# Kernel optimization log

Measured on AMD Instinct MI355X. Metric: run time of the kernel, lower is better.

## Reference

```python
import jax, jax.numpy as jnp
import numpy as np
import math

IN_FEATURES = 4096
OUT_FEATURES = 4096
TOKENS = 8192


def hydrate_weight(seed, out_features, in_features):
    """Deterministically synthesize the virtual weight matrix from the 64-bit seed.
    Mirrors nn.Linear's kaiming-uniform-style bound (1/sqrt(fan_in)) used by gmem_rs
    hydration; never stored as a parameter."""
    bound = 1.0 / math.sqrt(in_features)
    key = jax.random.key(seed)
    return jax.random.uniform(
        key, (out_features, in_features), dtype=jnp.float32,
        minval=-bound, maxval=bound)


def setup_inputs() -> dict:
    key = jax.random.key(0)
    kx, kb = jax.random.split(key)
    x = jax.random.normal(kx, (TOKENS, IN_FEATURES), dtype=jnp.float32)
    bound = 1.0 / math.sqrt(IN_FEATURES)
    bias = jax.random.uniform(kb, (OUT_FEATURES,), dtype=jnp.float32,
                              minval=-bound, maxval=bound)
    return {"x": x, "bias": bias, "seed": 1140071481}


def reference(x, bias, seed):
    # Hydrate weight on-the-fly from seed (zero-RAM virtual weight), then GEMM.
    W = hydrate_weight(seed, OUT_FEATURES, IN_FEATURES)  # [out, in]
    y = jnp.einsum('ti,oi->to', x, W)  # [tokens, out]
    return y + bias
```

## Files before the change

kernel.cpp:

```cpp
#include <hip/hip_runtime.h>
#include <hip/hip_bf16.h>
#include <stdint.h>

#define TOKENS 8192
#define NOUT   4096
#define KIN    4096

#define BM 256
#define BN 256
#define BK 64
#define NT (KIN / BK)

typedef __attribute__((ext_vector_type(8))) short bf16x8;
typedef __attribute__((ext_vector_type(4))) float f32x4;

__device__ __forceinline__ uint32_t rotl32(uint32_t x, int r) {
  return (x << r) | (x >> (32 - r));
}

__device__ __forceinline__ uint16_t f2bf_rne(float f) {
  uint32_t u = __float_as_uint(f);
  u += 0x7FFFu + ((u >> 16) & 1u);
  return (uint16_t)(u >> 16);
}

__device__ __forceinline__ void threefry2x32(uint32_t k0, uint32_t k1,
                                             uint32_t c0, uint32_t c1,
                                             uint32_t& o0, uint32_t& o1) {
  uint32_t ks2 = 0x1BD11BDAu ^ k0 ^ k1;
  uint32_t x0 = c0 + k0;
  uint32_t x1 = c1 + k1;
#define TFR(r) { x0 += x1; x1 = rotl32(x1, (r)); x1 ^= x0; }
  TFR(13) TFR(15) TFR(26) TFR(6)
  x0 += k1;  x1 += ks2 + 1u;
  TFR(17) TFR(29) TFR(16) TFR(24)
  x0 += ks2; x1 += k0 + 2u;
  TFR(13) TFR(15) TFR(26) TFR(6)
  x0 += k0;  x1 += k1 + 3u;
  TFR(17) TFR(29) TFR(16) TFR(24)
  x0 += k1;  x1 += ks2 + 4u;
  TFR(13) TFR(15) TFR(26) TFR(6)
  x0 += ks2; x1 += k0 + 5u;
#undef TFR
  o0 = x0; o1 = x1;
}

__global__ void prep_kernel(const float* __restrict__ x,
                            uint16_t* __restrict__ xb,
                            uint16_t* __restrict__ W,
                            const int* __restrict__ seed_ptr) {
  uint32_t b = blockIdx.x;
  if (b < 65536u) {
    uint32_t k1 = (uint32_t)(*seed_ptr);
    uint32_t j = b * 256u + threadIdx.x;
    uint32_t o0, o1;
    threefry2x32(0u, k1, 0u, j, o0, o1);
    uint32_t bits = o0 ^ o1;
    const float scale = 0.03125f;
    const float mn    = -0.015625f;
    float f = __uint_as_float((bits >> 9) | 0x3F800000u) - 1.0f;
    float v = fmaxf(mn, f * scale + mn);
    W[j] = f2bf_rne(v);
  } else {
    uint32_t base = ((b - 65536u) * 256u + threadIdx.x) * 8u;
    f32x4 a = *(const f32x4*)(x + base);
    f32x4 c = *(const f32x4*)(x + base + 4);
    union { uint16_t u[8]; bf16x8 v; } r;
    r.u[0] = f2bf_rne(a[0]); r.u[1] = f2bf_rne(a[1]);
    r.u[2] = f2bf_rne(a[2]); r.u[3] = f2bf_rne(a[3]);
    r.u[4] = f2bf_rne(c[0]); r.u[5] = f2bf_rne(c[1]);
    r.u[6] = f2bf_rne(c[2]); r.u[7] = f2bf_rne(c[3]);
    *(bf16x8*)(xb + base) = r.v;
  }
}

__global__ __launch_bounds__(512, 2)
void gemm_bias_kernel(const uint16_t* __restrict__ A,
                      const uint16_t* __restrict__ B,
                      const float* __restrict__ bias,
                      float* __restrict__ C) {
  __shared__ uint16_t smem[2][2][16384];

  const int nwgn = NOUT / BN;
  const int nwg  = (TOKENS / BM) * nwgn;
  int bid = blockIdx.x;
  int cpx = nwg >> 3;
  int swzb = (bid & 7) * cpx + (bid >> 3);
  int tm = (swzb / nwgn) * BM;
  int tn = (swzb % nwgn) * BN;

  const int t    = threadIdx.x;
  const int lane = t & 63;
  const int wid  = t >> 6;
  const int wm   = wid >> 2;
  const int wn   = wid & 3;
  const int fr   = lane & 15;
  const int fq   = lane >> 4;

  const int swzRd = (lane & 7) << 4;
  const int lsw   = ((lane & 7) ^ (lane >> 3)) << 4;

  f32x4 acc[8][4] = {};

  auto stageHalf = [&](int mat, int h, int kt, int buf) {
    const uint16_t* g = mat ? B : A;
    const int rb = (mat ? tn : tm) + h * 128 + wid * 16 + (lane >> 3);
    const char* src = (const char*)(g + (size_t)rb * KIN) + kt * 128 + lsw;
    char* dst = (char*)&smem[buf][mat][0] + h * 16384 + wid * 2048 + lane * 16;
#pragma unroll
    for (int q = 0; q < 2; ++q) {
      __builtin_amdgcn_global_load_lds(
          (const __attribute__((address_space(1))) void*)(src + (size_t)q * 8 * KIN * 2),
          (__attribute__((address_space(3))) void*)(dst + q * 1024),
          16, 0, 0);
    }
  };

#define VMW(N) asm volatile("s_waitcnt vmcnt(" #N ")" ::: "memory")
#define LKW(N) asm volatile("s_waitcnt lgkmcnt(" #N ")" ::: "memory")

#define RD_A(Ab, MH)                                                           \
    _Pragma("unroll")                                                          \
    for (int s = 0; s < 2; ++s) {                                              \
      const int kb = (s << 6) | (fq << 4);                                     \
      _Pragma("unroll")                                                        \
      for (int i = 0; i < 4; ++i)                                              \
        af[s][i] = *(const bf16x8*)((Ab) +                                     \
            (wm * 64 + (MH) * 128 + i * 16 + fr) * 128 + (kb ^ swzRd));        \
    }

#define RD_B(Bb, BV, NH)                                                       \
    _Pragma("unroll")                                                          \
    for (int s = 0; s < 2; ++s) {                                              \
      const int kb = (s << 6) | (fq << 4);                                     \
      _Pragma("unroll")                                                        \
      for (int j = 0; j < 2; ++j)                                              \
        BV[s][j] = *(const bf16x8*)((Bb) +                                     \
            (wn * 32 + (NH) * 128 + j * 16 + fr) * 128 + (kb ^ swzRd));        \
    }

#define MFCL(MH, NH, BV)                                                       \
    __builtin_amdgcn_s_barrier();                                              \
    asm volatile("s_waitcnt lgkmcnt(0)" ::: "memory");                         \
    __builtin_amdgcn_sched_barrier(0);                                         \
    __builtin_amdgcn_s_setprio(1);                                             \
    _Pragma("unroll")                                                          \
    for (int s = 0; s < 2; ++s)                                                \
      _Pragma("unroll")                                                        \
      for (int i = 0; i < 4; ++i)                                              \
        _Pragma("unroll")                                                      \
        for (int j = 0; j < 2; ++j)                                            \
          acc[(MH) * 4 + i][(NH) * 2 + j] =                                    \
              __builtin_amdgcn_mfma_f32_16x16x32_bf16(                         \
                  af[s][i], BV[s][j], acc[(MH) * 4 + i][(NH) * 2 + j], 0, 0, 0); \
    __builtin_amdgcn_s_setprio(0);                                             \
    __builtin_amdgcn_s_barrier();

#define KTILE(BUF, KT, MODE)                                                   \
  {                                                                            \
    bf16x8 af[2][4], bv0[2][2], bv1[2][2];                                     \
    const char* Ab = (const char*)&smem[BUF][0][0];                            \
    const char* Bb = (const char*)&smem[BUF][1][0];                            \
                              \
    RD_A(Ab, 0) RD_B(Bb, bv0, 0)                                               \
    if ((MODE) <= 1) stageHalf(0, 1, (KT) + 1, (BUF) ^ 1);                     \
    LKW(8);                                                                    \
    MFCL(0, 0, bv0)                                                            \
                                    \
    RD_B(Bb, bv1, 1)                                                           \
    if ((MODE) == 0) stageHalf(0, 0, (KT) + 2, (BUF));                         \
    MFCL(0, 1, bv1)                                                            \
                                    \
    RD_A(Ab, 1)                                                                \
    if ((MODE) == 0) stageHalf(1, 0, (KT) + 2, (BUF));                         \
    MFCL(1, 1, bv1)                                                            \
            \
    if ((MODE) == 0) stageHalf(1, 1, (KT) + 2, (BUF));                         \
    if ((MODE) == 0) { VMW(6); } else if ((MODE) == 1) { VMW(0); }             \
    MFCL(1, 0, bv0)                                                            \
  }

  stageHalf(0, 0, 0, 0); stageHalf(1, 0, 0, 0);
  stageHalf(0, 1, 0, 0); stageHalf(1, 1, 0, 0);
  VMW(4);
  stageHalf(0, 0, 1, 1); stageHalf(1, 0, 1, 1); stageHalf(1, 1, 1, 1);
  VMW(6);
  __builtin_amdgcn_s_barrier();

  for (int kt = 0; kt < NT - 2; kt += 2) {
    KTILE(0, kt, 0)
    KTILE(1, kt + 1, 0)
  }
  KTILE(0, 62, 1)
  KTILE(1, 63, 2)

#undef KTILE
#undef MFCL
#undef RD_B
#undef RD_A
#undef LKW
#undef VMW

#pragma unroll
  for (int nj = 0; nj < 4; ++nj) {
    const int nh = nj >> 1, j = nj & 1;
    const int col = tn + wn * 32 + nh * 128 + j * 16 + fr;
    const float bvs = bias[col];
#pragma unroll
    for (int mi = 0; mi < 8; ++mi) {
      const int mh = mi >> 2, i = mi & 3;
      const int row0 = tm + wm * 64 + mh * 128 + i * 16 + fq * 4;
#pragma unroll
      for (int rr = 0; rr < 4; ++rr)
        C[(size_t)(row0 + rr) * NOUT + col] = acc[mi][nj][rr] + bvs;
    }
  }
}

extern "C" void kernel_launch(void* const* d_in, const int* in_sizes, int n_in,
                              void* d_out, int out_size, void* d_ws, size_t ws_size,
                              hipStream_t stream) {
  const float* x    = (const float*)d_in[0];
  const float* bias = (const float*)d_in[1];
  const int*   seed = (const int*)d_in[2];
  float* y = (float*)d_out;

  uint16_t* Wb = (uint16_t*)d_ws;
  uint16_t* Xb = Wb + (size_t)NOUT * KIN;

  prep_kernel<<<65536 + 16384, 256, 0, stream>>>(x, Xb, Wb, seed);

  const int grid = (TOKENS / BM) * (NOUT / BN);
  gemm_bias_kernel<<<grid, 512, 0, stream>>>(Xb, Wb, bias, y);
}
```

Before: 284.1 us.

## Switch GEMM inner loop to 32x32x16 MFMA with split LDS reads

Replaces the 16x16x32 bf16 MFMA tiles with 32x32x16 MFMAs, so each wave issues fewer, larger matrix instructions and needs fewer LDS fragment reads per k-tile. LDS reads are split into two halves with partial lgkmcnt waits, so the first MFMA batch can start before all fragments arrive. The accumulator layout and epilogue indexing are remapped to the 32x32 output layout. The extra barriers and the changed register footprint could reduce overlap or occupancy.

```diff
diff --git a/kernel.cpp b/kernel.cpp
--- a/kernel.cpp
+++ b/kernel.cpp
@@ -11,8 +11,9 @@
 #define BK 64
 #define NT (KIN / BK)
 
-typedef __attribute__((ext_vector_type(8))) short bf16x8;
-typedef __attribute__((ext_vector_type(4))) float f32x4;
+typedef __attribute__((ext_vector_type(8)))  short bf16x8;
+typedef __attribute__((ext_vector_type(4)))  float f32x4;
+typedef __attribute__((ext_vector_type(16))) float f32x16;
 
 __device__ __forceinline__ uint32_t rotl32(uint32_t x, int r) {
   return (x << r) | (x >> (32 - r));
@@ -94,13 +95,13 @@
   const int wid  = t >> 6;
   const int wm   = wid >> 2;
   const int wn   = wid & 3;
-  const int fr   = lane & 15;
-  const int fq   = lane >> 4;
+  const int rrow = lane & 31;
+  const int khi  = (lane >> 5) << 4;
 
   const int swzRd = (lane & 7) << 4;
   const int lsw   = ((lane & 7) ^ (lane >> 3)) << 4;
 
-  f32x4 acc[8][4] = {};
+  f32x16 acc[4][2] = {};
 
   auto stageHalf = [&](int mat, int h, int kt, int buf) {
     const uint16_t* g = mat ? B : A;
@@ -118,66 +119,71 @@
 
 #define VMW(N) asm volatile("s_waitcnt vmcnt(" #N ")" ::: "memory")
 #define LKW(N) asm volatile("s_waitcnt lgkmcnt(" #N ")" ::: "memory")
-
-#define RD_A(Ab, MH)                                                           \
+#define SB0    __builtin_amdgcn_sched_barrier(0)
+#define PRI(p) __builtin_amdgcn_s_setprio(p)
+
+#define RD_A2(Ab, MH, S)                                                       \
     _Pragma("unroll")                                                          \
-    for (int s = 0; s < 2; ++s) {                                              \
-      const int kb = (s << 6) | (fq << 4);                                     \
+    for (int ss = 0; ss < 2; ++ss)                                             \
       _Pragma("unroll")                                                        \
-      for (int i = 0; i < 4; ++i)                                              \
-        af[s][i] = *(const bf16x8*)((Ab) +                                     \
-            (wm * 64 + (MH) * 128 + i * 16 + fr) * 128 + (kb ^ swzRd));        \
-    }
-
-#define RD_B(Bb, BV, NH)                                                       \
+      for (int i2 = 0; i2 < 2; ++i2)                                           \
+        af[(S) + ss][i2] = *(const bf16x8*)((Ab) +                             \
+            (wm * 64 + (MH) * 128 + i2 * 32 + rrow) * 128 +                    \
+            (((((S) + ss) << 5) + khi) ^ swzRd));
+
+#define RD_B2(Bb, BV, NH, S)                                                   \
     _Pragma("unroll")                                                          \
-    for (int s = 0; s < 2; ++s) {                                              \
-      const int kb = (s << 6) | (fq << 4);                                     \
+    for (int ss = 0; ss < 2; ++ss)                                             \
+      BV[(S) + ss] = *(const bf16x8*)((Bb) +                                   \
+          (wn * 32 + (NH) * 128 + rrow) * 128 +                                \
+          (((((S) + ss) << 5) + khi) ^ swzRd));
+
+#define MF4(MH, NH, BV, S)                                                     \
+    _Pragma("unroll")                                                          \
+    for (int ss = 0; ss < 2; ++ss)                                             \
       _Pragma("unroll")                                                        \
-      for (int j = 0; j < 2; ++j)                                              \
-        BV[s][j] = *(const bf16x8*)((Bb) +                                     \
-            (wn * 32 + (NH) * 128 + j * 16 + fr) * 128 + (kb ^ swzRd));        \
-    }
-
-#define MFCL(MH, NH, BV)                                                       \
-    __builtin_amdgcn_s_barrier();                                              \
-    asm volatile("s_waitcnt lgkmcnt(0)" ::: "memory");                         \
-    __builtin_amdgcn_sched_barrier(0);                                         \
-    __builtin_amdgcn_s_setprio(1);                                             \
-    _Pragma("unroll")                                                          \
-    for (int s = 0; s < 2; ++s)                                                \
-      _Pragma("unroll")                                                        \
-      for (int i = 0; i < 4; ++i)                                              \
-        _Pragma("unroll")                                                      \
-        for (int j = 0; j < 2; ++j)                                            \
-          acc[(MH) * 4 + i][(NH) * 2 + j] =                                    \
-              __builtin_amdgcn_mfma_f32_16x16x32_bf16(                         \
-                  af[s][i], BV[s][j], acc[(MH) * 4 + i][(NH) * 2 + j], 0, 0, 0); \
-    __builtin_amdgcn_s_setprio(0);                                             \
-    __builtin_amdgcn_s_barrier();
+      for (int i2 = 0; i2 < 2; ++i2)                                           \
+        acc[(MH) * 2 + i2][NH] = __builtin_amdgcn_mfma_f32_32x32x16_bf16(      \
+            af[(S) + ss][i2], BV[(S) + ss], acc[(MH) * 2 + i2][NH], 0, 0, 0);
 
 #define KTILE(BUF, KT, MODE)                                                   \
   {                                                                            \
-    bf16x8 af[2][4], bv0[2][2], bv1[2][2];                                     \
+    bf16x8 af[4][2], bv0[4], bv1[4];                                           \
     const char* Ab = (const char*)&smem[BUF][0][0];                            \
     const char* Bb = (const char*)&smem[BUF][1][0];                            \
-                              \
-    RD_A(Ab, 0) RD_B(Bb, bv0, 0)                                               \
+                  \
+    RD_A2(Ab, 0, 0) RD_B2(Bb, bv0, 0, 0)                                       \
+    SB0;                                                                       \
+    RD_A2(Ab, 0, 2) RD_B2(Bb, bv0, 0, 2)                                       \
     if ((MODE) <= 1) stageHalf(0, 1, (KT) + 1, (BUF) ^ 1);                     \
-    LKW(8);                                                                    \
-    MFCL(0, 0, bv0)                                                            \
-                                    \
-    RD_B(Bb, bv1, 1)                                                           \
+    __builtin_amdgcn_s_barrier();                                              \
+    LKW(6); SB0; PRI(1); MF4(0, 0, bv0, 0)                                     \
+    LKW(0); SB0; MF4(0, 0, bv0, 2) PRI(0);                                     \
+    __builtin_amdgcn_s_barrier();                                              \
+                       \
+    RD_B2(Bb, bv1, 1, 0)                                                       \
+    SB0;                                                                       \
+    RD_B2(Bb, bv1, 1, 2)                                                       \
     if ((MODE) == 0) stageHalf(0, 0, (KT) + 2, (BUF));                         \
-    MFCL(0, 1, bv1)                                                            \
-                                    \
-    RD_A(Ab, 1)                                                                \
+    __builtin_amdgcn_s_barrier();                                              \
+    LKW(2); SB0; PRI(1); MF4(0, 1, bv1, 0)                                     \
+    LKW(0); SB0; MF4(0, 1, bv1, 2) PRI(0);                                     \
+    __builtin_amdgcn_s_barrier();                                              \
+       \
+    RD_A2(Ab, 1, 0)                                                            \
+    SB0;                                                                       \
+    RD_A2(Ab, 1, 2)                                                            \
     if ((MODE) == 0) stageHalf(1, 0, (KT) + 2, (BUF));                         \
-    MFCL(1, 1, bv1)                                                            \
-            \
+    __builtin_amdgcn_s_barrier();                                              \
+    LKW(4); SB0; PRI(1); MF4(1, 1, bv1, 0)                                     \
+    LKW(0); SB0; MF4(1, 1, bv1, 2) PRI(0);                                     \
+    __builtin_amdgcn_s_barrier();                                              \
+       \
     if ((MODE) == 0) stageHalf(1, 1, (KT) + 2, (BUF));                         \
     if ((MODE) == 0) { VMW(6); } else if ((MODE) == 1) { VMW(0); }             \
-    MFCL(1, 0, bv0)                                                            \
+    __builtin_amdgcn_s_barrier();                                              \
+    PRI(1); MF4(1, 0, bv0, 0) MF4(1, 0, bv0, 2) PRI(0);                        \
+    __builtin_amdgcn_s_barrier();                                              \
   }
 
   stageHalf(0, 0, 0, 0); stageHalf(1, 0, 0, 0);
@@ -195,24 +201,27 @@
   KTILE(1, 63, 2)
 
 #undef KTILE
-#undef MFCL
-#undef RD_B
-#undef RD_A
+#undef MF4
+#undef RD_B2
+#undef RD_A2
+#undef PRI
+#undef SB0
 #undef LKW
 #undef VMW
 
 #pragma unroll
-  for (int nj = 0; nj < 4; ++nj) {
-    const int nh = nj >> 1, j = nj & 1;
-    const int col = tn + wn * 32 + nh * 128 + j * 16 + fr;
+  for (int nh = 0; nh < 2; ++nh) {
+    const int col = tn + wn * 32 + nh * 128 + rrow;
     const float bvs = bias[col];
 #pragma unroll
-    for (int mi = 0; mi < 8; ++mi) {
-      const int mh = mi >> 2, i = mi & 3;
-      const int row0 = tm + wm * 64 + mh * 128 + i * 16 + fq * 4;
-#pragma unroll
-      for (int rr = 0; rr < 4; ++rr)
-        C[(size_t)(row0 + rr) * NOUT + col] = acc[mi][nj][rr] + bvs;
+    for (int mi2 = 0; mi2 < 4; ++mi2) {
+      const int mh = mi2 >> 1, i2 = mi2 & 1;
+      const int row0 = tm + wm * 64 + mh * 128 + i2 * 32 + ((lane >> 5) << 2);
+#pragma unroll
+      for (int r = 0; r < 16; ++r) {
+        const int row = row0 + (r & 3) + 8 * (r >> 2);
+        C[(size_t)row * NOUT + col] = acc[mi2][nh][r] + bvs;
+      }
     }
   }
 }
```

After: 307.9 us. +8.4%, slower.

## Prefetch next k-tile's first LDS fragments during last MFMA cluster

Applied to the files above, without the earlier changes.

Restructures the per-k-tile schedule so the A/B fragments for the next tile's first MFMA cluster are read from LDS while the current tile's last cluster runs, with fragments held in persistent registers across tiles. It also reorders the MFMA quadrants and tunes lgkmcnt waits so LDS reads overlap the matrix-core work instead of stalling before each cluster. The cost is more live vector registers (two A and two B fragment sets), which may lower occupancy or cause spills, and the prologue now waits for all initial loads.

```diff
diff --git a/kernel.cpp b/kernel.cpp
--- a/kernel.cpp
+++ b/kernel.cpp
@@ -118,74 +118,79 @@
 
 #define VMW(N) asm volatile("s_waitcnt vmcnt(" #N ")" ::: "memory")
 #define LKW(N) asm volatile("s_waitcnt lgkmcnt(" #N ")" ::: "memory")
-
-#define RD_A(Ab, MH)                                                           \
+#define SB0    __builtin_amdgcn_sched_barrier(0)
+#define PRI(p) __builtin_amdgcn_s_setprio(p)
+
+#define RD_A(BUFI, AF, MH)                                                     \
     _Pragma("unroll")                                                          \
-    for (int s = 0; s < 2; ++s) {                                              \
-      const int kb = (s << 6) | (fq << 4);                                     \
+    for (int s_ = 0; s_ < 2; ++s_) {                                           \
+      const int kb_ = (s_ << 6) | (fq << 4);                                   \
       _Pragma("unroll")                                                        \
-      for (int i = 0; i < 4; ++i)                                              \
-        af[s][i] = *(const bf16x8*)((Ab) +                                     \
-            (wm * 64 + (MH) * 128 + i * 16 + fr) * 128 + (kb ^ swzRd));        \
-    }
-
-#define RD_B(Bb, BV, NH)                                                       \
+      for (int i_ = 0; i_ < 4; ++i_)                                           \
+        AF[s_][i_] = *(const bf16x8*)((const char*)&smem[BUFI][0][0] +         \
+            (wm * 64 + (MH) * 128 + i_ * 16 + fr) * 128 + (kb_ ^ swzRd));      \
+    }
+
+#define RD_B(BUFI, BV, NH)                                                     \
     _Pragma("unroll")                                                          \
-    for (int s = 0; s < 2; ++s) {                                              \
-      const int kb = (s << 6) | (fq << 4);                                     \
+    for (int s_ = 0; s_ < 2; ++s_) {                                           \
+      const int kb_ = (s_ << 6) | (fq << 4);                                   \
       _Pragma("unroll")                                                        \
-      for (int j = 0; j < 2; ++j)                                              \
-        BV[s][j] = *(const bf16x8*)((Bb) +                                     \
-            (wn * 32 + (NH) * 128 + j * 16 + fr) * 128 + (kb ^ swzRd));        \
-    }
-
-#define MFCL(MH, NH, BV)                                                       \
-    __builtin_amdgcn_s_barrier();                                              \
-    asm volatile("s_waitcnt lgkmcnt(0)" ::: "memory");                         \
-    __builtin_amdgcn_sched_barrier(0);                                         \
-    __builtin_amdgcn_s_setprio(1);                                             \
+      for (int j_ = 0; j_ < 2; ++j_)                                           \
+        BV[s_][j_] = *(const bf16x8*)((const char*)&smem[BUFI][1][0] +         \
+            (wn * 32 + (NH) * 128 + j_ * 16 + fr) * 128 + (kb_ ^ swzRd));      \
+    }
+
+#define MF16(MH, NH, AF, BV)                                                   \
     _Pragma("unroll")                                                          \
-    for (int s = 0; s < 2; ++s)                                                \
+    for (int s_ = 0; s_ < 2; ++s_)                                             \
       _Pragma("unroll")                                                        \
-      for (int i = 0; i < 4; ++i)                                              \
+      for (int i_ = 0; i_ < 4; ++i_)                                           \
         _Pragma("unroll")                                                      \
-        for (int j = 0; j < 2; ++j)                                            \
-          acc[(MH) * 4 + i][(NH) * 2 + j] =                                    \
+        for (int j_ = 0; j_ < 2; ++j_)                                         \
+          acc[(MH) * 4 + i_][(NH) * 2 + j_] =                                  \
               __builtin_amdgcn_mfma_f32_16x16x32_bf16(                         \
-                  af[s][i], BV[s][j], acc[(MH) * 4 + i][(NH) * 2 + j], 0, 0, 0); \
-    __builtin_amdgcn_s_setprio(0);                                             \
-    __builtin_amdgcn_s_barrier();
+                  AF[s_][i_], BV[s_][j_], acc[(MH) * 4 + i_][(NH) * 2 + j_],   \
+                  0, 0, 0);
 
 #define KTILE(BUF, KT, MODE)                                                   \
   {                                                                            \
-    bf16x8 af[2][4], bv0[2][2], bv1[2][2];                                     \
-    const char* Ab = (const char*)&smem[BUF][0][0];                            \
-    const char* Bb = (const char*)&smem[BUF][1][0];                            \
+             \
+    RD_B(BUF, bv1, 1)                                                          \
+    if ((MODE) <= 1) stageHalf(0, 1, (KT) + 1, (BUF) ^ 1);                     \
+    __builtin_amdgcn_s_barrier();                                              \
+    LKW(4); SB0; PRI(1); MF16(0, 0, af0, bv0) PRI(0);                          \
+    __builtin_amdgcn_s_barrier();                                              \
+               \
+    RD_A(BUF, af1, 1)                                                          \
+    if ((MODE) == 0) stageHalf(0, 0, (KT) + 2, (BUF));                         \
+    __builtin_amdgcn_s_barrier();                                              \
+    LKW(8); SB0; PRI(1); MF16(0, 1, af0, bv1) PRI(0);                          \
+    __builtin_amdgcn_s_barrier();                                              \
                               \
-    RD_A(Ab, 0) RD_B(Bb, bv0, 0)                                               \
-    if ((MODE) <= 1) stageHalf(0, 1, (KT) + 1, (BUF) ^ 1);                     \
-    LKW(8);                                                                    \
-    MFCL(0, 0, bv0)                                                            \
-                                    \
-    RD_B(Bb, bv1, 1)                                                           \
-    if ((MODE) == 0) stageHalf(0, 0, (KT) + 2, (BUF));                         \
-    MFCL(0, 1, bv1)                                                            \
-                                    \
-    RD_A(Ab, 1)                                                                \
     if ((MODE) == 0) stageHalf(1, 0, (KT) + 2, (BUF));                         \
-    MFCL(1, 1, bv1)                                                            \
-            \
+    __builtin_amdgcn_s_barrier();                                              \
+    LKW(0); SB0; PRI(1); MF16(1, 0, af1, bv0) PRI(0);                          \
+    __builtin_amdgcn_s_barrier();                                              \
+     \
+       \
     if ((MODE) == 0) stageHalf(1, 1, (KT) + 2, (BUF));                         \
     if ((MODE) == 0) { VMW(6); } else if ((MODE) == 1) { VMW(0); }             \
-    MFCL(1, 0, bv0)                                                            \
-  }
+    __builtin_amdgcn_s_barrier();                                              \
+    SB0;                                                                       \
+    PRI(1); MF16(1, 1, af1, bv1) PRI(0);                                       \
+    if ((MODE) <= 1) { RD_A((BUF) ^ 1, af0, 0) RD_B((BUF) ^ 1, bv0, 0) }       \
+    __builtin_amdgcn_s_barrier();                                              \
+  }
+
+  bf16x8 af0[2][4], af1[2][4], bv0[2][2], bv1[2][2];
 
   stageHalf(0, 0, 0, 0); stageHalf(1, 0, 0, 0);
-  stageHalf(0, 1, 0, 0); stageHalf(1, 1, 0, 0);
-  VMW(4);
+  stageHalf(1, 1, 0, 0); stageHalf(0, 1, 0, 0);
+  VMW(0);
+  __builtin_amdgcn_s_barrier();
+  RD_A(0, af0, 0) RD_B(0, bv0, 0)
   stageHalf(0, 0, 1, 1); stageHalf(1, 0, 1, 1); stageHalf(1, 1, 1, 1);
-  VMW(6);
-  __builtin_amdgcn_s_barrier();
 
   for (int kt = 0; kt < NT - 2; kt += 2) {
     KTILE(0, kt, 0)
@@ -195,9 +200,11 @@
   KTILE(1, 63, 2)
 
 #undef KTILE
-#undef MFCL
+#undef MF16
 #undef RD_B
 #undef RD_A
+#undef PRI
+#undef SB0
 #undef LKW
 #undef VMW
 
```

New measurement: 425.5 us. +49.8%, slower.
